# Optimization experiments

Measured on AMD Instinct MI355X. Metric: run time of the kernel, lower is better.

## Reference

```python
import jax, jax.numpy as jnp
import numpy as np

N, E = 50000, 800000
IN_C, HID, OUT_C = 128, 128, 64
EPS = 1e-5


def layer_norm(x, gamma, beta):
    mu = jnp.mean(x, axis=-1, keepdims=True)
    var = jnp.mean(jnp.square(x - mu), axis=-1, keepdims=True)
    return (x - mu) * jax.lax.rsqrt(var + EPS) * gamma + beta


def sage_conv(h, src, dst, W_l, b_l, W_r):
    # PyG SAGEConv (aggr='mean'): out = lin_l(mean_{j in N(i)} h_j) + lin_r(h_i)
    msg = h[src]                                                   # [E, HID] gather
    s = jax.ops.segment_sum(msg, dst, num_segments=N)              # [N, HID]
    cnt = jax.ops.segment_sum(jnp.ones((src.shape[0], 1), h.dtype), dst, num_segments=N)
    mean = s / jnp.maximum(cnt, 1.0)
    return mean @ W_l + b_l + h @ W_r


def setup_inputs() -> dict:
    key = jax.random.key(0)
    ks = jax.random.split(key, 12)
    sd_in = 1.0 / np.sqrt(IN_C)
    sd_h = 1.0 / np.sqrt(HID)
    return {
        "x": jax.random.normal(ks[0], (N, IN_C), jnp.float32),
        "edge_index": jax.random.randint(ks[1], (2, E), 0, N, jnp.int32),
        "edge_attr": jax.random.normal(ks[2], (E, IN_C), jnp.float32),
        "W_ne": jax.random.uniform(ks[3], (IN_C, HID), jnp.float32, -sd_in, sd_in),
        "b_ne": jax.random.uniform(ks[4], (HID,), jnp.float32, -sd_in, sd_in),
        "W_l": jax.random.uniform(ks[5], (HID, HID), jnp.float32, -sd_h, sd_h),
        "b_l": jax.random.uniform(ks[6], (HID,), jnp.float32, -sd_h, sd_h),
        "W_r": jax.random.uniform(ks[7], (HID, HID), jnp.float32, -sd_h, sd_h),
        "gamma": jnp.ones((HID,), jnp.float32),
        "beta": jnp.zeros((HID,), jnp.float32),
        "W_lin": jax.random.uniform(ks[8], (HID, OUT_C), jnp.float32, -sd_h, sd_h),
        "b_lin": jax.random.uniform(ks[9], (OUT_C,), jnp.float32, -sd_h, sd_h),
    }


def reference(x, edge_index, edge_attr, W_ne, b_ne, W_l, b_l, W_r, gamma, beta, W_lin, b_lin):
    src, dst = edge_index[0], edge_index[1]
    # node encoder
    h = x @ W_ne + b_ne
    # pre-conv with layers[0].conv
    h = sage_conv(h, src, dst, W_l, b_l, W_r)
    # layers[0] is unfixed: LN -> ReLU -> dropout(eval=id) -> conv -> residual
    r = layer_norm(h, gamma, beta)
    r = jax.nn.relu(r)
    h = sage_conv(r, src, dst, W_l, b_l, W_r) + h
    # layers[1:] are fixed -> identity
    # final norm/act/dropout(eval=id)/lin (reuses layers[0].norm/act)
    o = jax.nn.relu(layer_norm(h, gamma, beta))
    return o @ W_lin + b_lin
```

## Files before the change

### kernel.cpp

```cpp
#include <hip/hip_runtime.h>

typedef __attribute__((ext_vector_type(8))) short bf16x8;
typedef __attribute__((ext_vector_type(4))) float f32x4;

constexpr float LN_EPS = 1e-5f;

__device__ inline ushort f2bf(float f) {
  uint u = __float_as_uint(f);
  u += 0x7FFF + ((u >> 16) & 1);
  return (ushort)(u >> 16);
}
__device__ inline float bflo(uint u) { return __uint_as_float(u << 16); }
__device__ inline float bfhi(uint u) { return __uint_as_float(u & 0xFFFF0000u); }
__device__ inline uint pk2(float lo, float hi) { return (uint)f2bf(lo) | ((uint)f2bf(hi) << 16); }

struct Params {
  const float* x; const int* ei;
  const float *W_ne, *b_ne, *W_l, *b_l, *W_r, *gamma, *beta, *W_lin, *b_lin;
  float* out;
  ushort *Abf, *Qbf, *H1, *Dbf, *xbf, *WAt, *WBt, *Wlt, *Wrt, *Wlint;
  float *bA, *bB;
  int *cnt, *incl, *rowptr, *cursor, *bsums, *srclist;
  int N, E, nbS, nbT;
};


__global__ __launch_bounds__(256) void k_hist(Params p) {
  int e = blockIdx.x * 256 + threadIdx.x;
  if (e < p.E) atomicAdd(&p.cnt[p.ei[p.E + e]], 1);
}

__global__ __launch_bounds__(256) void k_p2(Params p) {
  __shared__ int sh[256];
  const int tid = threadIdx.x, bid = blockIdx.x;
  if (bid < p.nbS) {
    int i = bid * 256 + tid;
    int v = (i < p.N) ? p.cnt[i] : 0;
    sh[tid] = v;
    __syncthreads();
    for (int off = 1; off < 256; off <<= 1) {
      int t = (tid >= off) ? sh[tid - off] : 0;
      __syncthreads();
      sh[tid] += t;
      __syncthreads();
    }
    if (i < p.N) p.incl[i] = sh[tid];
    if (tid == 255) p.bsums[bid] = sh[255];
  } else if (bid < p.nbS + 129) {
    int blk = bid - p.nbS;
    float* srow = (float*)sh;
    const float* src = (blk < 128) ? (p.W_ne + blk * 128) : p.b_ne;
    if (tid < 128) srow[tid] = src[tid];
    __syncthreads();
    int col = tid & 127;
    const float* Wx = (tid < 128) ? p.W_l : p.W_r;
    float acc = 0.f;
#pragma unroll 8
    for (int k = 0; k < 128; ++k) acc = fmaf(srow[k], Wx[k * 128 + col], acc);
    if (blk < 128) {
      ushort* dst = (tid < 128) ? p.WAt : p.WBt;
      dst[col * 128 + blk] = f2bf(acc);
    } else {
      float* dst = (tid < 128) ? p.bA : p.bB;
      dst[col] = acc;
    }
  } else {
    const int nx16 = p.N * 16;
    const int total = nx16 + 16384 + 16384 + 8192;
    const int i0 = (bid - (p.nbS + 129)) * 256 + tid;
    const int st = (gridDim.x - (p.nbS + 129)) * 256;
    const float4* xin = (const float4*)p.x;
    uint4* xo = (uint4*)p.xbf;
    for (int idx = i0; idx < total; idx += st) {
      if (idx < nx16) {
        float4 a = xin[2 * (size_t)idx], b = xin[2 * (size_t)idx + 1];
        uint4 v;
        v.x = pk2(a.x, a.y); v.y = pk2(a.z, a.w);
        v.z = pk2(b.x, b.y); v.w = pk2(b.z, b.w);
        xo[idx] = v;
        continue;
      }
      int t = idx - nx16;
      if (t < 16384) { p.Wlt[(t & 127) * 128 + (t >> 7)] = f2bf(p.W_l[t]); continue; }
      t -= 16384;
      if (t < 16384) { p.Wrt[(t & 127) * 128 + (t >> 7)] = f2bf(p.W_r[t]); continue; }
      t -= 16384;
      p.Wlint[(t & 63) * 128 + (t >> 6)] = f2bf(p.W_lin[t]);
    }
  }
}

__global__ __launch_bounds__(256) void k_scan2(Params p) {
  __shared__ int sh[256];
  const int tid = threadIdx.x;
  int v = (tid < p.nbS) ? p.bsums[tid] : 0;
  sh[tid] = v;
  __syncthreads();
  for (int off = 1; off < 256; off <<= 1) {
    int t = (tid >= off) ? sh[tid - off] : 0;
    __syncthreads();
    sh[tid] += t;
    __syncthreads();
  }
  if (tid < p.nbS) p.bsums[tid] = sh[tid] - v;
}

__global__ __launch_bounds__(256) void k_fill(Params p) {
  int e = blockIdx.x * 256 + threadIdx.x;
  if (e >= p.E) return;
  int s = p.ei[e], d = p.ei[p.E + e];
  int pos = atomicAdd(&p.cursor[d], 1);
  p.srclist[pos] = s;
}


template <int NCOL, bool BF16OUT>
__device__ __forceinline__ void gemm_tile(const ushort* __restrict__ X, const ushort* __restrict__ Wt,
                                          const float* __restrict__ bias, void* __restrict__ Yv,
                                          int M, int tile) {
  constexpr int NF = NCOL / 32;
  const int tid = threadIdx.x;
  const int wave = tid >> 6, lane = tid & 63;
  const int rbase = (wave >> 1) * 64;
  const int cbase = (wave & 1) * (NCOL / 2);
  const int lrow = lane & 15;
  const int lkb = (lane >> 4) * 8;
  const int row0 = tile * 128;

  size_t rIdx[4];
#pragma unroll
  for (int mf = 0; mf < 4; ++mf) {
    int r = row0 + rbase + mf * 16 + lrow;
    rIdx[mf] = (size_t)((r < M) ? r : (M - 1));
  }

  f32x4 acc[4][NF];
#pragma unroll
  for (int mf = 0; mf < 4; ++mf)
#pragma unroll
    for (int nf = 0; nf < NF; ++nf) acc[mf][nf] = (f32x4){0.f, 0.f, 0.f, 0.f};

#pragma unroll
  for (int ks = 0; ks < 4; ++ks) {
    bf16x8 a[4], b[NF];
#pragma unroll
    for (int mf = 0; mf < 4; ++mf)
      a[mf] = *(const bf16x8*)(X + rIdx[mf] * 128 + ks * 32 + lkb);
#pragma unroll
    for (int nf = 0; nf < NF; ++nf)
      b[nf] = *(const bf16x8*)(Wt + (size_t)(cbase + nf * 16 + lrow) * 128 + ks * 32 + lkb);
#pragma unroll
    for (int mf = 0; mf < 4; ++mf)
#pragma unroll
      for (int nf = 0; nf < NF; ++nf)
        acc[mf][nf] = __builtin_amdgcn_mfma_f32_16x16x32_bf16(a[mf], b[nf], acc[mf][nf], 0, 0, 0);
  }

#pragma unroll
  for (int nf = 0; nf < NF; ++nf) {
    int col = cbase + nf * 16 + lrow;
    float bv = bias ? bias[col] : 0.f;
#pragma unroll
    for (int mf = 0; mf < 4; ++mf) {
      int growb = row0 + rbase + mf * 16 + (lane >> 4) * 4;
#pragma unroll
      for (int r = 0; r < 4; ++r) {
        int grow = growb + r;
        if (grow < M) {
          float val = acc[mf][nf][r] + bv;
          if constexpr (BF16OUT)
            ((ushort*)Yv)[(size_t)grow * NCOL + col] = f2bf(val);
          else
            ((float*)Yv)[(size_t)grow * NCOL + col] = val;
        }
      }
    }
  }
}

__global__ __launch_bounds__(256) void k_p4(Params p) {
  const int bid = blockIdx.x, tid = threadIdx.x;
  if (bid < p.nbS) {
    int i = bid * 256 + tid;
    if (i < p.N) {
      int inc = p.incl[i] + p.bsums[bid];
      p.rowptr[i + 1] = inc;
      p.cursor[i] = inc - p.cnt[i];
    }
    if (i == 0) p.rowptr[0] = 0;
    return;
  }
  int job = bid - p.nbS;
  if (job < p.nbT) gemm_tile<128, true>(p.xbf, p.WAt, p.bA, p.Abf, p.N, job);
  else gemm_tile<128, true>(p.xbf, p.WBt, p.bB, p.Qbf, p.N, job - p.nbT);
}

__global__ __launch_bounds__(256) void k_gemm2(Params p) {
  int job = blockIdx.y * p.nbT + blockIdx.x;
  if (job < p.nbT) gemm_tile<128, true>(p.Dbf, p.Wlt, nullptr, p.Abf, p.N, job);
  else gemm_tile<128, true>(p.Dbf, p.Wrt, nullptr, p.Qbf, p.N, job - p.nbT);
}

__global__ __launch_bounds__(256) void k_gout(Params p) {
  gemm_tile<64, false>(p.Dbf, p.Wlint, p.b_lin, p.out, p.N, blockIdx.x);
}


__device__ __forceinline__ void acc8(uint4 u, float* a) {
  a[0] += bflo(u.x); a[1] += bfhi(u.x);
  a[2] += bflo(u.y); a[3] += bfhi(u.y);
  a[4] += bflo(u.z); a[5] += bfhi(u.z);
  a[6] += bflo(u.w); a[7] += bfhi(u.w);
}

__device__ __forceinline__ void gather_mean(const ushort* __restrict__ Pm, const int* __restrict__ rowptr,
                                            const int* __restrict__ srclist, int w, int lane, float* a) {
  const uint4* Pv = (const uint4*)Pm;
  int fl = lane & 15, g4 = lane >> 4;
  int beg = rowptr[w], end = rowptr[w + 1];
  for (int base = beg; base < end; base += 64) {
    int m = end - base;
    if (m > 64) m = 64;
    int sidx = (lane < m) ? srclist[base + lane] : 0;
    for (int i = 0; i < m; i += 16) {
      int j0 = i + g4, j1 = j0 + 4, j2 = j0 + 8, j3 = j0 + 12;
      int s0 = __shfl(sidx, j0 & 63, 64);
      int s1 = __shfl(sidx, j1 & 63, 64);
      int s2 = __shfl(sidx, j2 & 63, 64);
      int s3 = __shfl(sidx, j3 & 63, 64);
      uint4 u0 = Pv[(size_t)s0 * 16 + fl];
      uint4 u1 = Pv[(size_t)s1 * 16 + fl];
      uint4 u2 = Pv[(size_t)s2 * 16 + fl];
      uint4 u3 = Pv[(size_t)s3 * 16 + fl];
      if (j0 < m) acc8(u0, a);
      if (j1 < m) acc8(u1, a);
      if (j2 < m) acc8(u2, a);
      if (j3 < m) acc8(u3, a);
    }
  }
#pragma unroll
  for (int k = 0; k < 8; ++k) {
    a[k] += __shfl_xor(a[k], 16, 64);
    a[k] += __shfl_xor(a[k], 32, 64);
  }
  float inv = 1.f / fmaxf((float)(end - beg), 1.f);
#pragma unroll
  for (int k = 0; k < 8; ++k) a[k] *= inv;
}

__device__ __forceinline__ void ln_relu8(const float* h, const float* __restrict__ gamma,
                                         const float* __restrict__ beta, int fl, float* o) {
  float sum = 0.f;
#pragma unroll
  for (int k = 0; k < 8; ++k) sum += h[k];
#pragma unroll
  for (int off = 1; off < 16; off <<= 1) sum += __shfl_xor(sum, off, 64);
  float mu = sum * (1.f / 128.f);
  float s2 = 0.f;
#pragma unroll
  for (int k = 0; k < 8; ++k) { float d = h[k] - mu; s2 += d * d; }
#pragma unroll
  for (int off = 1; off < 16; off <<= 1) s2 += __shfl_xor(s2, off, 64);
  float scale = rsqrtf(s2 * (1.f / 128.f) + LN_EPS);
  float4 g0 = *(const float4*)(gamma + fl * 8);
  float4 g1 = *(const float4*)(gamma + fl * 8 + 4);
  float4 b0 = *(const float4*)(beta + fl * 8);
  float4 b1 = *(const float4*)(beta + fl * 8 + 4);
  float gg[8] = {g0.x, g0.y, g0.z, g0.w, g1.x, g1.y, g1.z, g1.w};
  float bb[8] = {b0.x, b0.y, b0.z, b0.w, b1.x, b1.y, b1.z, b1.w};
#pragma unroll
  for (int k = 0; k < 8; ++k) o[k] = fmaxf((h[k] - mu) * scale * gg[k] + bb[k], 0.f);
}

__device__ __forceinline__ uint4 pack8(const float* v) {
  uint4 u;
  u.x = pk2(v[0], v[1]); u.y = pk2(v[2], v[3]);
  u.z = pk2(v[4], v[5]); u.w = pk2(v[6], v[7]);
  return u;
}

__global__ __launch_bounds__(256) void k_agg1(Params p) {
  int w = (blockIdx.x * 256 + threadIdx.x) >> 6;
  int lane = threadIdx.x & 63;
  if (w >= p.N) return;
  int fl = lane & 15;
  float a[8] = {0.f, 0.f, 0.f, 0.f, 0.f, 0.f, 0.f, 0.f};
  gather_mean(p.Abf, p.rowptr, p.srclist, w, lane, a);
  uint4 qv = ((const uint4*)p.Qbf)[(size_t)w * 16 + fl];
  float4 bl0 = *(const float4*)(p.b_l + fl * 8);
  float4 bl1 = *(const float4*)(p.b_l + fl * 8 + 4);
  float q[8] = {bflo(qv.x), bfhi(qv.x), bflo(qv.y), bfhi(qv.y), bflo(qv.z), bfhi(qv.z), bflo(qv.w), bfhi(qv.w)};
  float bl[8] = {bl0.x, bl0.y, bl0.z, bl0.w, bl1.x, bl1.y, bl1.z, bl1.w};
  float h[8];
#pragma unroll
  for (int k = 0; k < 8; ++k) h[k] = a[k] + q[k] + bl[k];
  float r[8];
  ln_relu8(h, p.gamma, p.beta, fl, r);
  if (lane < 16) {
    ((uint4*)p.H1)[(size_t)w * 16 + fl] = pack8(h);
    ((uint4*)p.Dbf)[(size_t)w * 16 + fl] = pack8(r);
  }
}

__global__ __launch_bounds__(256) void k_agg2(Params p) {
  int w = (blockIdx.x * 256 + threadIdx.x) >> 6;
  int lane = threadIdx.x & 63;
  if (w >= p.N) return;
  int fl = lane & 15;
  float a[8] = {0.f, 0.f, 0.f, 0.f, 0.f, 0.f, 0.f, 0.f};
  gather_mean(p.Abf, p.rowptr, p.srclist, w, lane, a);
  uint4 vv = ((const uint4*)p.Qbf)[(size_t)w * 16 + fl];
  uint4 hv = ((const uint4*)p.H1)[(size_t)w * 16 + fl];
  float4 bl0 = *(const float4*)(p.b_l + fl * 8);
  float4 bl1 = *(const float4*)(p.b_l + fl * 8 + 4);
  float vf[8] = {bflo(vv.x), bfhi(vv.x), bflo(vv.y), bfhi(vv.y), bflo(vv.z), bfhi(vv.z), bflo(vv.w), bfhi(vv.w)};
  float hf[8] = {bflo(hv.x), bfhi(hv.x), bflo(hv.y), bfhi(hv.y), bflo(hv.z), bfhi(hv.z), bflo(hv.w), bfhi(hv.w)};
  float bl[8] = {bl0.x, bl0.y, bl0.z, bl0.w, bl1.x, bl1.y, bl1.z, bl1.w};
  float h[8];
#pragma unroll
  for (int k = 0; k < 8; ++k) h[k] = a[k] + vf[k] + bl[k] + hf[k];
  float o[8];
  ln_relu8(h, p.gamma, p.beta, fl, o);
  if (lane < 16) ((uint4*)p.Dbf)[(size_t)w * 16 + fl] = pack8(o);
}


extern "C" void kernel_launch(void* const* d_in, const int* in_sizes, int n_in,
                              void* d_out, int out_size, void* d_ws, size_t ws_size,
                              hipStream_t stream) {
  Params p;
  p.x = (const float*)d_in[0];
  p.ei = (const int*)d_in[1];
  p.W_ne = (const float*)d_in[3];
  p.b_ne = (const float*)d_in[4];
  p.W_l = (const float*)d_in[5];
  p.b_l = (const float*)d_in[6];
  p.W_r = (const float*)d_in[7];
  p.gamma = (const float*)d_in[8];
  p.beta = (const float*)d_in[9];
  p.W_lin = (const float*)d_in[10];
  p.b_lin = (const float*)d_in[11];
  p.out = (float*)d_out;

  p.N = in_sizes[0] / 128;
  p.E = in_sizes[1] / 2;
  p.nbS = (p.N + 255) / 256;
  p.nbT = (p.N + 127) / 128;

  char* w = (char*)d_ws;
  const size_t S2 = (size_t)p.N * 128 * sizeof(ushort);
  p.Abf = (ushort*)w;    w += S2;
  p.Qbf = (ushort*)w;    w += S2;
  p.H1 = (ushort*)w;     w += S2;
  p.Dbf = (ushort*)w;    w += S2;
  p.xbf = (ushort*)w;    w += S2;
  p.WAt = (ushort*)w;    w += 128 * 128 * sizeof(ushort);
  p.WBt = (ushort*)w;    w += 128 * 128 * sizeof(ushort);
  p.Wlt = (ushort*)w;    w += 128 * 128 * sizeof(ushort);
  p.Wrt = (ushort*)w;    w += 128 * 128 * sizeof(ushort);
  p.Wlint = (ushort*)w;  w += 64 * 128 * sizeof(ushort);
  p.bA = (float*)w;      w += 128 * sizeof(float);
  p.bB = (float*)w;      w += 128 * sizeof(float);
  p.cnt = (int*)w;       w += (size_t)p.N * sizeof(int);
  p.incl = (int*)w;      w += (size_t)p.N * sizeof(int);
  p.rowptr = (int*)w;    w += ((size_t)p.N + 4) * sizeof(int);
  p.cursor = (int*)w;    w += (size_t)p.N * sizeof(int);
  p.bsums = (int*)w;     w += 1024 * sizeof(int);
  p.srclist = (int*)w;

  const int nbE = (p.E + 255) / 256;
  const int nbW = ((p.N * 64) + 255) / 256;

  hipMemsetAsync(p.cnt, 0, (size_t)p.N * sizeof(int), stream);
  k_hist<<<nbE, 256, 0, stream>>>(p);
  k_p2<<<p.nbS + 129 + 1024, 256, 0, stream>>>(p);
  k_scan2<<<1, 256, 0, stream>>>(p);
  k_p4<<<p.nbS + 2 * p.nbT, 256, 0, stream>>>(p);
  k_fill<<<nbE, 256, 0, stream>>>(p);
  k_agg1<<<nbW, 256, 0, stream>>>(p);
  k_gemm2<<<dim3(p.nbT, 2), 256, 0, stream>>>(p);
  k_agg2<<<nbW, 256, 0, stream>>>(p);
  k_gout<<<p.nbT, 256, 0, stream>>>(p);
}
```

Baseline: 241.6 us.

## Quantize gathered message features to int8 with per-row scales; fold block scan into p4

The projected neighbour features that the aggregation kernels gather are now stored as int8 with one fp32 scale per row. The GEMM epilogue computes each row's absolute max through LDS and writes the quantized tile. This halves the bytes moved by the random gather over 800k edges, at the cost of accuracy loss from int8 quantization and an extra scale load per edge. Separately, the single-block scan kernel is removed, and each scan block now reduces the preceding block sums itself, saving one kernel launch.

```diff
diff --git a/kernel.cpp b/kernel.cpp
--- a/kernel.cpp
+++ b/kernel.cpp
@@ -18,7 +18,9 @@
   const float* x; const int* ei;
   const float *W_ne, *b_ne, *W_l, *b_l, *W_r, *gamma, *beta, *W_lin, *b_lin;
   float* out;
-  ushort *Abf, *Qbf, *H1, *Dbf, *xbf, *WAt, *WBt, *Wlt, *Wrt, *Wlint;
+  ushort *Qbf, *H1, *Dbf, *xbf, *WAt, *WBt, *Wlt, *Wrt, *Wlint;
+  signed char* Aq;
+  float* Ascale;
   float *bA, *bB;
   int *cnt, *incl, *rowptr, *cursor, *bsums, *srclist;
   int N, E, nbS, nbT;
@@ -90,21 +92,6 @@
   }
 }
 
-__global__ __launch_bounds__(256) void k_scan2(Params p) {
-  __shared__ int sh[256];
-  const int tid = threadIdx.x;
-  int v = (tid < p.nbS) ? p.bsums[tid] : 0;
-  sh[tid] = v;
-  __syncthreads();
-  for (int off = 1; off < 256; off <<= 1) {
-    int t = (tid >= off) ? sh[tid - off] : 0;
-    __syncthreads();
-    sh[tid] += t;
-    __syncthreads();
-  }
-  if (tid < p.nbS) p.bsums[tid] = sh[tid] - v;
-}
-
 __global__ __launch_bounds__(256) void k_fill(Params p) {
   int e = blockIdx.x * 256 + threadIdx.x;
   if (e >= p.E) return;
@@ -114,10 +101,10 @@
 }
 
 
-template <int NCOL, bool BF16OUT>
+template <int NCOL, int OMODE>
 __device__ __forceinline__ void gemm_tile(const ushort* __restrict__ X, const ushort* __restrict__ Wt,
                                           const float* __restrict__ bias, void* __restrict__ Yv,
-                                          int M, int tile) {
+                                          float* __restrict__ Yscale, int M, int tile, char* ldsraw) {
   constexpr int NF = NCOL / 32;
   const int tid = threadIdx.x;
   const int wave = tid >> 6, lane = tid & 63;
@@ -156,10 +143,61 @@
         acc[mf][nf] = __builtin_amdgcn_mfma_f32_16x16x32_bf16(a[mf], b[nf], acc[mf][nf], 0, 0, 0);
   }
 
+  if (bias) {
+#pragma unroll
+    for (int nf = 0; nf < NF; ++nf) {
+      float bv = bias[cbase + nf * 16 + lrow];
+#pragma unroll
+      for (int mf = 0; mf < 4; ++mf)
+#pragma unroll
+        for (int r = 0; r < 4; ++r) acc[mf][nf][r] += bv;
+    }
+  }
+
+  if constexpr (OMODE == 2) {
+    float (*rmaxh)[2] = (float(*)[2])ldsraw;
+    signed char (*qt)[128] = (signed char(*)[128])(ldsraw + 1024);
+#pragma unroll
+    for (int mf = 0; mf < 4; ++mf)
+#pragma unroll
+      for (int r = 0; r < 4; ++r) {
+        float m = 0.f;
+#pragma unroll
+        for (int nf = 0; nf < NF; ++nf) m = fmaxf(m, fabsf(acc[mf][nf][r]));
+#pragma unroll
+        for (int off = 1; off < 16; off <<= 1) m = fmaxf(m, __shfl_xor(m, off, 64));
+        int lr = rbase + mf * 16 + (lane >> 4) * 4 + r;
+        if (lrow == 0) rmaxh[lr][wave & 1] = m;
+      }
+    __syncthreads();
+#pragma unroll
+    for (int mf = 0; mf < 4; ++mf)
+#pragma unroll
+      for (int r = 0; r < 4; ++r) {
+        int lr = rbase + mf * 16 + (lane >> 4) * 4 + r;
+        float mx = fmaxf(rmaxh[lr][0], rmaxh[lr][1]);
+        float inv = (mx > 0.f) ? 127.f / mx : 0.f;
+#pragma unroll
+        for (int nf = 0; nf < NF; ++nf)
+          qt[lr][cbase + nf * 16 + lrow] = (signed char)__float2int_rn(acc[mf][nf][r] * inv);
+      }
+    __syncthreads();
+    signed char* Yq = (signed char*)Yv;
+    for (int idx = tid; idx < 1024; idx += 256) {
+      int lr = idx >> 3, co = (idx & 7) * 16;
+      int grow = row0 + lr;
+      if (grow < M) *(uint4*)(Yq + (size_t)grow * 128 + co) = *(const uint4*)&qt[lr][co];
+    }
+    if (tid < 128) {
+      int grow = row0 + tid;
+      if (grow < M) Yscale[grow] = fmaxf(rmaxh[tid][0], rmaxh[tid][1]) * (1.f / 127.f);
+    }
+    return;
+  }
+
 #pragma unroll
   for (int nf = 0; nf < NF; ++nf) {
     int col = cbase + nf * 16 + lrow;
-    float bv = bias ? bias[col] : 0.f;
 #pragma unroll
     for (int mf = 0; mf < 4; ++mf) {
       int growb = row0 + rbase + mf * 16 + (lane >> 4) * 4;
@@ -167,8 +205,8 @@
       for (int r = 0; r < 4; ++r) {
         int grow = growb + r;
         if (grow < M) {
-          float val = acc[mf][nf][r] + bv;
-          if constexpr (BF16OUT)
+          float val = acc[mf][nf][r];
+          if constexpr (OMODE == 1)
             ((ushort*)Yv)[(size_t)grow * NCOL + col] = f2bf(val);
           else
             ((float*)Yv)[(size_t)grow * NCOL + col] = val;
@@ -179,11 +217,21 @@
 }
 
 __global__ __launch_bounds__(256) void k_p4(Params p) {
+  __shared__ __align__(16) char qlds[1024 + 16384];
   const int bid = blockIdx.x, tid = threadIdx.x;
   if (bid < p.nbS) {
+    int* ss = (int*)qlds;
+    int v = (tid < bid) ? p.bsums[tid] : 0;
+    ss[tid] = v;
+    __syncthreads();
+    for (int off = 128; off > 0; off >>= 1) {
+      if (tid < off) ss[tid] += ss[tid + off];
+      __syncthreads();
+    }
+    int prefix = ss[0];
     int i = bid * 256 + tid;
     if (i < p.N) {
-      int inc = p.incl[i] + p.bsums[bid];
+      int inc = p.incl[i] + prefix;
       p.rowptr[i + 1] = inc;
       p.cursor[i] = inc - p.cnt[i];
     }
@@ -191,31 +239,36 @@
     return;
   }
   int job = bid - p.nbS;
-  if (job < p.nbT) gemm_tile<128, true>(p.xbf, p.WAt, p.bA, p.Abf, p.N, job);
-  else gemm_tile<128, true>(p.xbf, p.WBt, p.bB, p.Qbf, p.N, job - p.nbT);
+  if (job < p.nbT) gemm_tile<128, 2>(p.xbf, p.WAt, p.bA, p.Aq, p.Ascale, p.N, job, qlds);
+  else gemm_tile<128, 1>(p.xbf, p.WBt, p.bB, p.Qbf, nullptr, p.N, job - p.nbT, qlds);
 }
 
 __global__ __launch_bounds__(256) void k_gemm2(Params p) {
+  __shared__ __align__(16) char qlds[1024 + 16384];
   int job = blockIdx.y * p.nbT + blockIdx.x;
-  if (job < p.nbT) gemm_tile<128, true>(p.Dbf, p.Wlt, nullptr, p.Abf, p.N, job);
-  else gemm_tile<128, true>(p.Dbf, p.Wrt, nullptr, p.Qbf, p.N, job - p.nbT);
+  if (job < p.nbT) gemm_tile<128, 2>(p.Dbf, p.Wlt, nullptr, p.Aq, p.Ascale, p.N, job, qlds);
+  else gemm_tile<128, 1>(p.Dbf, p.Wrt, nullptr, p.Qbf, nullptr, p.N, job - p.nbT, qlds);
 }
 
 __global__ __launch_bounds__(256) void k_gout(Params p) {
-  gemm_tile<64, false>(p.Dbf, p.Wlint, p.b_lin, p.out, p.N, blockIdx.x);
-}
-
-
-__device__ __forceinline__ void acc8(uint4 u, float* a) {
-  a[0] += bflo(u.x); a[1] += bfhi(u.x);
-  a[2] += bflo(u.y); a[3] += bfhi(u.y);
-  a[4] += bflo(u.z); a[5] += bfhi(u.z);
-  a[6] += bflo(u.w); a[7] += bfhi(u.w);
-}
-
-__device__ __forceinline__ void gather_mean(const ushort* __restrict__ Pm, const int* __restrict__ rowptr,
-                                            const int* __restrict__ srclist, int w, int lane, float* a) {
-  const uint4* Pv = (const uint4*)Pm;
+  gemm_tile<64, 0>(p.Dbf, p.Wlint, p.b_lin, p.out, nullptr, p.N, blockIdx.x, nullptr);
+}
+
+
+__device__ __forceinline__ void acc8q(uint2 u, float sc, float* a) {
+  a[0] = fmaf((float)(int)(signed char)(u.x & 0xFF), sc, a[0]);
+  a[1] = fmaf((float)(int)(signed char)((u.x >> 8) & 0xFF), sc, a[1]);
+  a[2] = fmaf((float)(int)(signed char)((u.x >> 16) & 0xFF), sc, a[2]);
+  a[3] = fmaf((float)(int)(signed char)(u.x >> 24), sc, a[3]);
+  a[4] = fmaf((float)(int)(signed char)(u.y & 0xFF), sc, a[4]);
+  a[5] = fmaf((float)(int)(signed char)((u.y >> 8) & 0xFF), sc, a[5]);
+  a[6] = fmaf((float)(int)(signed char)((u.y >> 16) & 0xFF), sc, a[6]);
+  a[7] = fmaf((float)(int)(signed char)(u.y >> 24), sc, a[7]);
+}
+
+__device__ __forceinline__ void gather_mean(const signed char* __restrict__ Pq, const float* __restrict__ Psc,
+                                            const int* __restrict__ rowptr, const int* __restrict__ srclist,
+                                            int w, int lane, float* a) {
   int fl = lane & 15, g4 = lane >> 4;
   int beg = rowptr[w], end = rowptr[w + 1];
   for (int base = beg; base < end; base += 64) {
@@ -228,14 +281,15 @@
       int s1 = __shfl(sidx, j1 & 63, 64);
       int s2 = __shfl(sidx, j2 & 63, 64);
       int s3 = __shfl(sidx, j3 & 63, 64);
-      uint4 u0 = Pv[(size_t)s0 * 16 + fl];
-      uint4 u1 = Pv[(size_t)s1 * 16 + fl];
-      uint4 u2 = Pv[(size_t)s2 * 16 + fl];
-      uint4 u3 = Pv[(size_t)s3 * 16 + fl];
-      if (j0 < m) acc8(u0, a);
-      if (j1 < m) acc8(u1, a);
-      if (j2 < m) acc8(u2, a);
-      if (j3 < m) acc8(u3, a);
+      float c0 = Psc[s0], c1 = Psc[s1], c2 = Psc[s2], c3 = Psc[s3];
+      uint2 u0 = *(const uint2*)(Pq + (size_t)s0 * 128 + fl * 8);
+      uint2 u1 = *(const uint2*)(Pq + (size_t)s1 * 128 + fl * 8);
+      uint2 u2 = *(const uint2*)(Pq + (size_t)s2 * 128 + fl * 8);
+      uint2 u3 = *(const uint2*)(Pq + (size_t)s3 * 128 + fl * 8);
+      if (j0 < m) acc8q(u0, c0, a);
+      if (j1 < m) acc8q(u1, c1, a);
+      if (j2 < m) acc8q(u2, c2, a);
+      if (j3 < m) acc8q(u3, c3, a);
     }
   }
 #pragma unroll
@@ -285,7 +339,7 @@
   if (w >= p.N) return;
   int fl = lane & 15;
   float a[8] = {0.f, 0.f, 0.f, 0.f, 0.f, 0.f, 0.f, 0.f};
-  gather_mean(p.Abf, p.rowptr, p.srclist, w, lane, a);
+  gather_mean(p.Aq, p.Ascale, p.rowptr, p.srclist, w, lane, a);
   uint4 qv = ((const uint4*)p.Qbf)[(size_t)w * 16 + fl];
   float4 bl0 = *(const float4*)(p.b_l + fl * 8);
   float4 bl1 = *(const float4*)(p.b_l + fl * 8 + 4);
@@ -308,7 +362,7 @@
   if (w >= p.N) return;
   int fl = lane & 15;
   float a[8] = {0.f, 0.f, 0.f, 0.f, 0.f, 0.f, 0.f, 0.f};
-  gather_mean(p.Abf, p.rowptr, p.srclist, w, lane, a);
+  gather_mean(p.Aq, p.Ascale, p.rowptr, p.srclist, w, lane, a);
   uint4 vv = ((const uint4*)p.Qbf)[(size_t)w * 16 + fl];
   uint4 hv = ((const uint4*)p.H1)[(size_t)w * 16 + fl];
   float4 bl0 = *(const float4*)(p.b_l + fl * 8);
@@ -349,11 +403,12 @@
 
   char* w = (char*)d_ws;
   const size_t S2 = (size_t)p.N * 128 * sizeof(ushort);
-  p.Abf = (ushort*)w;    w += S2;
   p.Qbf = (ushort*)w;    w += S2;
   p.H1 = (ushort*)w;     w += S2;
   p.Dbf = (ushort*)w;    w += S2;
   p.xbf = (ushort*)w;    w += S2;
+  p.Aq = (signed char*)w;  w += (size_t)p.N * 128;
+  p.Ascale = (float*)w;  w += (size_t)p.N * sizeof(float);
   p.WAt = (ushort*)w;    w += 128 * 128 * sizeof(ushort);
   p.WBt = (ushort*)w;    w += 128 * 128 * sizeof(ushort);
   p.Wlt = (ushort*)w;    w += 128 * 128 * sizeof(ushort);
@@ -374,7 +429,6 @@
   hipMemsetAsync(p.cnt, 0, (size_t)p.N * sizeof(int), stream);
   k_hist<<<nbE, 256, 0, stream>>>(p);
   k_p2<<<p.nbS + 129 + 1024, 256, 0, stream>>>(p);
-  k_scan2<<<1, 256, 0, stream>>>(p);
   k_p4<<<p.nbS + 2 * p.nbT, 256, 0, stream>>>(p);
   k_fill<<<nbE, 256, 0, stream>>>(p);
   k_agg1<<<nbW, 256, 0, stream>>>(p);
```

Result: faster. 224.8 us (-6.9%).
